# Kernel optimization log

Hardware: AMD Instinct MI355X
Metric: run time of the kernel (lower is better)

## Reference

```python
import jax, jax.numpy as jnp
import numpy as np

PROCESSING_SPEED = 8.0  # init kwarg: softmax temperature
EPS = 1e-8              # torch F.cosine_similarity eps
BATCH, SIZE, DIM = 1024, 65536, 512


def setup_inputs() -> dict:
    key = jax.random.key(0)
    k1, k2 = jax.random.split(key)
    x = jax.random.normal(k1, (BATCH, DIM), dtype=jnp.float32)
    memory_bank = jax.random.normal(k2, (SIZE, DIM), dtype=jnp.float32)
    return {"x": x, "memory_bank": memory_bank}


def reference(x, memory_bank):
    # Cosine similarity between every query and every memory row, computed as
    # normalized dot products (math-equivalent to F.cosine_similarity with
    # denominator clamp max(||a||*||b||, eps), avoiding the (B,S,D) broadcast).
    x_norm = jnp.linalg.norm(x, axis=1, keepdims=True)            # (B, 1)
    m_norm = jnp.linalg.norm(memory_bank, axis=1, keepdims=True)  # (S, 1)
    dots = jnp.einsum('bd,sd->bs', x, memory_bank)                # (B, S)
    sims = dots / jnp.maximum(x_norm * m_norm.T, EPS)             # (B, S)
    attention = jax.nn.softmax(sims * PROCESSING_SPEED, axis=1)   # (B, S)
    return attention @ memory_bank                                # (B, D)
```

## Files before the change

### kernel.cpp

```cpp
#include <hip/hip_runtime.h>
#include <hip/hip_bf16.h>
#include <stdint.h>

#define B_N 1024
#define S_N 65536
#define D_N 512
#define SCALE 8.0f
#define KSPLIT 32
#define KCHUNK (S_N / KSPLIT)

typedef __attribute__((ext_vector_type(8))) short bf16x8;
typedef __attribute__((ext_vector_type(4))) float f32x4;
typedef __attribute__((ext_vector_type(4))) unsigned int u32x4;

#define OFF_MBF   ((size_t)0)
#define OFF_MT    (OFF_MBF + (size_t)S_N * D_N * 2)
#define OFF_XBF   (OFF_MT  + (size_t)D_N * S_N * 2)
#define OFF_P     (OFF_XBF + (size_t)B_N * D_N * 2)
#define OFF_XNSQ  (OFF_P   + (size_t)B_N * S_N * 2)
#define OFF_MNSQ  (OFF_XNSQ + (size_t)B_N * 4)
#define OFF_LSUM  (OFF_MNSQ + (size_t)S_N * 4)
#define OFF_OPART OFF_MBF

__device__ __forceinline__ unsigned short f2bf(float f) {
  unsigned u = __builtin_bit_cast(unsigned, f);
  u += 0x7fffu + ((u >> 16) & 1u);
  return (unsigned short)(u >> 16);
}

__device__ __forceinline__ void stage16(const unsigned short* g, unsigned short* l) {
  __builtin_amdgcn_global_load_lds(
      (const __attribute__((address_space(1))) void*)g,
      (__attribute__((address_space(3))) void*)l, 16, 0, 0);
}

__global__ void k_prep_x(const float* __restrict__ X, unsigned short* __restrict__ Xbf,
                         float* __restrict__ xnsq) {
  const int row = blockIdx.x;
  const int t = threadIdx.x;
  float4 v = ((const float4*)(X + (size_t)row * D_N))[t];
  float ss = v.x*v.x + v.y*v.y + v.z*v.z + v.w*v.w;
  ushort4 o; o.x = f2bf(v.x); o.y = f2bf(v.y); o.z = f2bf(v.z); o.w = f2bf(v.w);
  ((ushort4*)(Xbf + (size_t)row * D_N))[t] = o;
  #pragma unroll
  for (int m = 1; m < 64; m <<= 1) ss += __shfl_xor(ss, m);
  __shared__ float partial[2];
  if ((t & 63) == 0) partial[t >> 6] = ss;
  __syncthreads();
  if (t == 0) xnsq[row] = partial[0] + partial[1];
}

__global__ void k_prep_m(const float* __restrict__ M, unsigned short* __restrict__ Mbf,
                         unsigned short* __restrict__ Mt, float* __restrict__ mnsq) {
  __shared__ float ts[64 * 65];
  const int t = threadIdx.x;
  const int s0 = blockIdx.x * 64;
  const int r = t >> 2, cq = t & 3;
  const int c = t >> 2, sq = t & 3;
  float ss = 0.f;
  for (int ct = 0; ct < 8; ++ct) {
    float f[16];
    const float4* src = (const float4*)(M + (size_t)(s0 + r) * D_N + ct * 64 + cq * 16);
    #pragma unroll
    for (int k = 0; k < 4; ++k) {
      float4 v = src[k];
      f[4*k+0] = v.x; f[4*k+1] = v.y; f[4*k+2] = v.z; f[4*k+3] = v.w;
    }
    union { unsigned short u[16]; uint4 v4[2]; } pk;
    #pragma unroll
    for (int j = 0; j < 16; ++j) {
      ss += f[j] * f[j];
      pk.u[j] = f2bf(f[j]);
      ts[r * 65 + cq * 16 + j] = f[j];
    }
    uint4* dst = (uint4*)(Mbf + (size_t)(s0 + r) * D_N + ct * 64 + cq * 16);
    dst[0] = pk.v4[0]; dst[1] = pk.v4[1];
    __syncthreads();
    union { unsigned short u[16]; u32x4 v4[2]; } pt;
    #pragma unroll
    for (int j = 0; j < 16; ++j) pt.u[j] = f2bf(ts[(sq * 16 + j) * 65 + c]);
    u32x4* dt = (u32x4*)(Mt + (size_t)(ct * 64 + c) * S_N + s0 + sq * 16);
    __builtin_nontemporal_store(pt.v4[0], dt + 0);
    __builtin_nontemporal_store(pt.v4[1], dt + 1);
    __syncthreads();
  }
  ss += __shfl_xor(ss, 1);
  ss += __shfl_xor(ss, 2);
  if (cq == 0) mnsq[s0 + r] = ss;
}

__global__ __launch_bounds__(256, 4) void k_qk(
    const unsigned short* __restrict__ Xbf, const unsigned short* __restrict__ Mbf,
    const float* __restrict__ xnsq, const float* __restrict__ mnsq,
    unsigned short* __restrict__ P, float* __restrict__ lsum) {
  __shared__ unsigned short As[128 * 64];
  __shared__ unsigned short Bs[128 * 64];
  const int t = threadIdx.x;
  const int w = t >> 6, lane = t & 63, quad = lane >> 4, l15 = lane & 15;
  const int wr = w >> 1, wc = w & 1;
  const int x7 = l15 & 7;
  const int flat = blockIdx.x;
  const int xcd = flat & 7, sl = flat >> 3;
  const int bn = xcd * 64 + (sl >> 3);
  const int bm = sl & 7;

  f32x4 acc[4][4];
  #pragma unroll
  for (int i = 0; i < 4; ++i)
    #pragma unroll
    for (int j = 0; j < 4; ++j) acc[i][j] = (f32x4){0.f, 0.f, 0.f, 0.f};

  const int srow = t >> 3;
  const int schunk = (t & 7) ^ (srow & 7);
  const unsigned short* gA = Xbf + (size_t)(bm * 128 + srow) * D_N + schunk * 8;
  const unsigned short* gB = Mbf + (size_t)(bn * 128 + srow) * D_N + schunk * 8;
  unsigned short* lA = As + w * 512;
  unsigned short* lB = Bs + w * 512;

  for (int k0 = 0; k0 < D_N; k0 += 64) {
    #pragma unroll
    for (int i = 0; i < 4; ++i) {
      stage16(gA + (size_t)(i * 32) * D_N + k0, lA + i * 2048);
      stage16(gB + (size_t)(i * 32) * D_N + k0, lB + i * 2048);
    }
    __syncthreads();
    #pragma unroll
    for (int kk = 0; kk < 64; kk += 32) {
      const int cq = (kk >> 3) + quad;
      bf16x8 af[4], bfr[4];
      #pragma unroll
      for (int i = 0; i < 4; ++i)
        af[i] = *(const bf16x8*)&As[(wr * 64 + i * 16 + l15) * 64 + (cq ^ x7) * 8];
      #pragma unroll
      for (int j = 0; j < 4; ++j)
        bfr[j] = *(const bf16x8*)&Bs[(wc * 64 + j * 16 + l15) * 64 + (cq ^ x7) * 8];
      #pragma unroll
      for (int i = 0; i < 4; ++i)
        #pragma unroll
        for (int j = 0; j < 4; ++j)
          acc[i][j] = __builtin_amdgcn_mfma_f32_16x16x32_bf16(af[i], bfr[j], acc[i][j], 0, 0, 0);
    }
    __syncthreads();
  }

  float mn_[4];
  #pragma unroll
  for (int j = 0; j < 4; ++j) mn_[j] = mnsq[bn * 128 + wc * 64 + j * 16 + l15];
  #pragma unroll
  for (int i = 0; i < 4; ++i) {
    float rowsum[4];
    #pragma unroll
    for (int r = 0; r < 4; ++r) {
      const int b = bm * 128 + wr * 64 + i * 16 + quad * 4 + r;
      const float xq = xnsq[b];
      float rs = 0.f;
      #pragma unroll
      for (int j = 0; j < 4; ++j) {
        float d2 = fmaxf(xq * mn_[j], 1e-16f);
        float p = __expf(SCALE * acc[i][j][r] * rsqrtf(d2));
        rs += p;
        const int s = bn * 128 + wc * 64 + j * 16 + l15;
        P[(size_t)b * S_N + s] = f2bf(p);
      }
      rowsum[r] = rs;
    }
    #pragma unroll
    for (int r = 0; r < 4; ++r) {
      float rs = rowsum[r];
      rs += __shfl_xor(rs, 1);
      rs += __shfl_xor(rs, 2);
      rs += __shfl_xor(rs, 4);
      rs += __shfl_xor(rs, 8);
      if (l15 == 0) {
        const int b = bm * 128 + wr * 64 + i * 16 + quad * 4 + r;
        unsafeAtomicAdd(&lsum[b], rs);
      }
    }
  }
}

__global__ __launch_bounds__(256, 4) void k_pv(
    const unsigned short* __restrict__ P, const unsigned short* __restrict__ Mt,
    float* __restrict__ Opart) {
  __shared__ unsigned short As[128 * 64];
  __shared__ unsigned short Bs[128 * 64];
  const int t = threadIdx.x;
  const int w = t >> 6, lane = t & 63, quad = lane >> 4, l15 = lane & 15;
  const int wr = w >> 1, wc = w & 1;
  const int x7 = l15 & 7;
  const int flat = blockIdx.x;
  const int xcd = flat & 7, sl = flat >> 3;
  const int ks = xcd * 4 + (sl >> 5);
  const int rem = sl & 31;
  const int bn = rem >> 3, bm = rem & 7;

  f32x4 acc[4][4];
  #pragma unroll
  for (int i = 0; i < 4; ++i)
    #pragma unroll
    for (int j = 0; j < 4; ++j) acc[i][j] = (f32x4){0.f, 0.f, 0.f, 0.f};

  const int srow = t >> 3;
  const int schunk = (t & 7) ^ (srow & 7);
  const unsigned short* gA = P  + (size_t)(bm * 128 + srow) * S_N + (size_t)ks * KCHUNK + schunk * 8;
  const unsigned short* gB = Mt + (size_t)(bn * 128 + srow) * S_N + (size_t)ks * KCHUNK + schunk * 8;
  unsigned short* lA = As + w * 512;
  unsigned short* lB = Bs + w * 512;

  for (int k0 = 0; k0 < KCHUNK; k0 += 64) {
    #pragma unroll
    for (int i = 0; i < 4; ++i) {
      stage16(gA + (size_t)(i * 32) * S_N + k0, lA + i * 2048);
      stage16(gB + (size_t)(i * 32) * S_N + k0, lB + i * 2048);
    }
    __syncthreads();
    #pragma unroll
    for (int kk = 0; kk < 64; kk += 32) {
      const int cq = (kk >> 3) + quad;
      bf16x8 af[4], bfr[4];
      #pragma unroll
      for (int i = 0; i < 4; ++i)
        af[i] = *(const bf16x8*)&As[(wr * 64 + i * 16 + l15) * 64 + (cq ^ x7) * 8];
      #pragma unroll
      for (int j = 0; j < 4; ++j)
        bfr[j] = *(const bf16x8*)&Bs[(wc * 64 + j * 16 + l15) * 64 + (cq ^ x7) * 8];
      #pragma unroll
      for (int i = 0; i < 4; ++i)
        #pragma unroll
        for (int j = 0; j < 4; ++j)
          acc[i][j] = __builtin_amdgcn_mfma_f32_16x16x32_bf16(af[i], bfr[j], acc[i][j], 0, 0, 0);
    }
    __syncthreads();
  }

  float* Od = Opart + (size_t)ks * (B_N * D_N);
  #pragma unroll
  for (int i = 0; i < 4; ++i)
    #pragma unroll
    for (int r = 0; r < 4; ++r) {
      const int b = bm * 128 + wr * 64 + i * 16 + quad * 4 + r;
      #pragma unroll
      for (int j = 0; j < 4; ++j) {
        const int d = bn * 128 + wc * 64 + j * 16 + l15;
        Od[(size_t)b * D_N + d] = acc[i][j][r];
      }
    }
}

__global__ void k_combine(const float* __restrict__ Opart, const float* __restrict__ lsum,
                          float* __restrict__ out) {
  const int idx = blockIdx.x * 256 + threadIdx.x;
  const int b = idx >> 7;
  float4 s = {0.f, 0.f, 0.f, 0.f};
  #pragma unroll
  for (int ks = 0; ks < KSPLIT; ++ks) {
    float4 v = ((const float4*)Opart)[(size_t)ks * (B_N * D_N / 4) + idx];
    s.x += v.x; s.y += v.y; s.z += v.z; s.w += v.w;
  }
  const float inv = 1.0f / lsum[b];
  s.x *= inv; s.y *= inv; s.z *= inv; s.w *= inv;
  ((float4*)out)[idx] = s;
}

extern "C" void kernel_launch(void* const* d_in, const int* in_sizes, int n_in,
                              void* d_out, int out_size, void* d_ws, size_t ws_size,
                              hipStream_t stream) {
  const float* X = (const float*)d_in[0];
  const float* M = (const float*)d_in[1];
  char* ws = (char*)d_ws;
  unsigned short* Mbf  = (unsigned short*)(ws + OFF_MBF);
  unsigned short* Mt   = (unsigned short*)(ws + OFF_MT);
  unsigned short* Xbf  = (unsigned short*)(ws + OFF_XBF);
  unsigned short* P    = (unsigned short*)(ws + OFF_P);
  float* xnsq = (float*)(ws + OFF_XNSQ);
  float* mnsq = (float*)(ws + OFF_MNSQ);
  float* lsum = (float*)(ws + OFF_LSUM);
  float* Opart = (float*)(ws + OFF_OPART);

  (void)hipMemsetAsync(lsum, 0, B_N * sizeof(float), stream);
  k_prep_x<<<dim3(B_N), 128, 0, stream>>>(X, Xbf, xnsq);
  k_prep_m<<<dim3(S_N / 64), 256, 0, stream>>>(M, Mbf, Mt, mnsq);
  k_qk<<<dim3(8 * (S_N / 128)), 256, 0, stream>>>(Xbf, Mbf, xnsq, mnsq, P, lsum);
  k_pv<<<dim3((D_N / 128) * (B_N / 128) * KSPLIT), 256, 0, stream>>>(P, Mt, Opart);
  k_combine<<<dim3(B_N * D_N / 4 / 256), 256, 0, stream>>>(Opart, lsum, (float*)d_out);
}
```

Measured before the change: 510.4 us.

## Stage QK softmax tile in LDS for coalesced P stores; precompute reciprocal norms

The QK epilogue now writes the exponentiated bf16 probabilities into an LDS tile, reusing the operand buffers, one 64-row half at a time. The tile is then copied to global memory with 16-byte coalesced row stores, replacing scattered 2-byte stores. The prep kernels store rsqrt of the squared norms, so the epilogue needs only multiplies instead of a per-element rsqrt. This adds two block barriers per half and leaves half the warps idle during each epilogue half, and the eps clamp on the norm product is dropped.

```diff
diff --git a/kernel.cpp b/kernel.cpp
--- a/kernel.cpp
+++ b/kernel.cpp
@@ -35,7 +35,7 @@
 }
 
 __global__ void k_prep_x(const float* __restrict__ X, unsigned short* __restrict__ Xbf,
-                         float* __restrict__ xnsq) {
+                         float* __restrict__ rsx) {
   const int row = blockIdx.x;
   const int t = threadIdx.x;
   float4 v = ((const float4*)(X + (size_t)row * D_N))[t];
@@ -47,11 +47,11 @@
   __shared__ float partial[2];
   if ((t & 63) == 0) partial[t >> 6] = ss;
   __syncthreads();
-  if (t == 0) xnsq[row] = partial[0] + partial[1];
+  if (t == 0) rsx[row] = rsqrtf(partial[0] + partial[1]);
 }
 
 __global__ void k_prep_m(const float* __restrict__ M, unsigned short* __restrict__ Mbf,
-                         unsigned short* __restrict__ Mt, float* __restrict__ mnsq) {
+                         unsigned short* __restrict__ Mt, float* __restrict__ rsm) {
   __shared__ float ts[64 * 65];
   const int t = threadIdx.x;
   const int s0 = blockIdx.x * 64;
@@ -86,15 +86,18 @@
   }
   ss += __shfl_xor(ss, 1);
   ss += __shfl_xor(ss, 2);
-  if (cq == 0) mnsq[s0 + r] = ss;
-}
-
+  if (cq == 0) rsm[s0 + r] = rsqrtf(ss);
+}
+
+#define PS_STRIDE 136
 __global__ __launch_bounds__(256, 4) void k_qk(
     const unsigned short* __restrict__ Xbf, const unsigned short* __restrict__ Mbf,
-    const float* __restrict__ xnsq, const float* __restrict__ mnsq,
+    const float* __restrict__ rsx, const float* __restrict__ rsm,
     unsigned short* __restrict__ P, float* __restrict__ lsum) {
-  __shared__ unsigned short As[128 * 64];
-  __shared__ unsigned short Bs[128 * 64];
+  __shared__ __align__(16) unsigned char smem[32768];
+  unsigned short* As = (unsigned short*)smem;
+  unsigned short* Bs = (unsigned short*)(smem + 16384);
+  unsigned short* Ps = (unsigned short*)smem;
   const int t = threadIdx.x;
   const int w = t >> 6, lane = t & 63, quad = lane >> 4, l15 = lane & 15;
   const int wr = w >> 1, wc = w & 1;
@@ -143,39 +146,48 @@
     __syncthreads();
   }
 
-  float mn_[4];
-  #pragma unroll
-  for (int j = 0; j < 4; ++j) mn_[j] = mnsq[bn * 128 + wc * 64 + j * 16 + l15];
-  #pragma unroll
-  for (int i = 0; i < 4; ++i) {
-    float rowsum[4];
-    #pragma unroll
-    for (int r = 0; r < 4; ++r) {
-      const int b = bm * 128 + wr * 64 + i * 16 + quad * 4 + r;
-      const float xq = xnsq[b];
-      float rs = 0.f;
-      #pragma unroll
-      for (int j = 0; j < 4; ++j) {
-        float d2 = fmaxf(xq * mn_[j], 1e-16f);
-        float p = __expf(SCALE * acc[i][j][r] * rsqrtf(d2));
-        rs += p;
-        const int s = bn * 128 + wc * 64 + j * 16 + l15;
-        P[(size_t)b * S_N + s] = f2bf(p);
+  float rm_[4];
+  #pragma unroll
+  for (int j = 0; j < 4; ++j) rm_[j] = rsm[bn * 128 + wc * 64 + j * 16 + l15];
+
+  #pragma unroll
+  for (int half = 0; half < 2; ++half) {
+    if (wr == half) {
+      #pragma unroll
+      for (int i = 0; i < 4; ++i) {
+        #pragma unroll
+        for (int r = 0; r < 4; ++r) {
+          const int lrow = i * 16 + quad * 4 + r;
+          const int b = bm * 128 + half * 64 + lrow;
+          const float srx = SCALE * rsx[b];
+          float rs = 0.f;
+          #pragma unroll
+          for (int j = 0; j < 4; ++j) {
+            float p = __expf(acc[i][j][r] * srx * rm_[j]);
+            rs += p;
+            Ps[lrow * PS_STRIDE + wc * 64 + j * 16 + l15] = f2bf(p);
+          }
+          rs += __shfl_xor(rs, 1);
+          rs += __shfl_xor(rs, 2);
+          rs += __shfl_xor(rs, 4);
+          rs += __shfl_xor(rs, 8);
+          if (l15 == 0) unsafeAtomicAdd(&lsum[b], rs);
+        }
       }
-      rowsum[r] = rs;
-    }
-    #pragma unroll
-    for (int r = 0; r < 4; ++r) {
-      float rs = rowsum[r];
-      rs += __shfl_xor(rs, 1);
-      rs += __shfl_xor(rs, 2);
-      rs += __shfl_xor(rs, 4);
-      rs += __shfl_xor(rs, 8);
-      if (l15 == 0) {
-        const int b = bm * 128 + wr * 64 + i * 16 + quad * 4 + r;
-        unsafeAtomicAdd(&lsum[b], rs);
-      }
-    }
+    }
+    __syncthreads();
+    {
+      const int row = t >> 2, c4 = t & 3;
+      const int gb = bm * 128 + half * 64 + row;
+      const unsigned short* src = &Ps[row * PS_STRIDE + c4 * 32];
+      uint4 v[4];
+      #pragma unroll
+      for (int k = 0; k < 4; ++k) v[k] = *(const uint4*)(src + k * 8);
+      uint4* dst = (uint4*)&P[(size_t)gb * S_N + bn * 128 + c4 * 32];
+      #pragma unroll
+      for (int k = 0; k < 4; ++k) dst[k] = v[k];
+    }
+    __syncthreads();
   }
 }
 
@@ -272,15 +284,15 @@
   unsigned short* Mt   = (unsigned short*)(ws + OFF_MT);
   unsigned short* Xbf  = (unsigned short*)(ws + OFF_XBF);
   unsigned short* P    = (unsigned short*)(ws + OFF_P);
-  float* xnsq = (float*)(ws + OFF_XNSQ);
-  float* mnsq = (float*)(ws + OFF_MNSQ);
+  float* rsx = (float*)(ws + OFF_XNSQ);
+  float* rsm = (float*)(ws + OFF_MNSQ);
   float* lsum = (float*)(ws + OFF_LSUM);
   float* Opart = (float*)(ws + OFF_OPART);
 
   (void)hipMemsetAsync(lsum, 0, B_N * sizeof(float), stream);
-  k_prep_x<<<dim3(B_N), 128, 0, stream>>>(X, Xbf, xnsq);
-  k_prep_m<<<dim3(S_N / 64), 256, 0, stream>>>(M, Mbf, Mt, mnsq);
-  k_qk<<<dim3(8 * (S_N / 128)), 256, 0, stream>>>(Xbf, Mbf, xnsq, mnsq, P, lsum);
+  k_prep_x<<<dim3(B_N), 128, 0, stream>>>(X, Xbf, rsx);
+  k_prep_m<<<dim3(S_N / 64), 256, 0, stream>>>(M, Mbf, Mt, rsm);
+  k_qk<<<dim3(8 * (S_N / 128)), 256, 0, stream>>>(Xbf, Mbf, rsx, rsm, P, lsum);
   k_pv<<<dim3((D_N / 128) * (B_N / 128) * KSPLIT), 256, 0, stream>>>(P, Mt, Opart);
   k_combine<<<dim3(B_N * D_N / 4 / 256), 256, 0, stream>>>(Opart, lsum, (float*)d_out);
 }
```

Result: slower. 553.5 us (+8.5%).
